# Optimization experiments

Hardware: AMD Instinct MI355X
Metric: run time of the kernel (lower is better)

## Reference

```python
import jax, jax.numpy as jnp
from jax import lax
import numpy as np

FILTER_SIZE = 3
PAD = FILTER_SIZE // 2


def _smooth(off, filt):
    # ReflectionPad2d(pad) -> conv2d(padding=pad) -> crop pad:-pad  == same-size smoothing
    x = jnp.pad(off, ((0, 0), (0, 0), (PAD, PAD), (PAD, PAD)), mode='reflect')
    y = lax.conv_general_dilated(x, filt, window_strides=(1, 1),
                                 padding=[(PAD, PAD), (PAD, PAD)],
                                 dimension_numbers=('NCHW', 'OIHW', 'NCHW'))
    return y[:, :, PAD:-PAD, PAD:-PAD]


def _grid_sample(img, gx, gy):
    # img: [C,H,W]; gx,gy: [N,H,W] normalized to [-1,1].
    # Bilinear, align_corners=True, zero padding (torch 1.x default at repo time).
    C, H, W = img.shape
    ix = (gx + 1.0) * 0.5 * (W - 1)
    iy = (gy + 1.0) * 0.5 * (H - 1)
    x0 = jnp.floor(ix); y0 = jnp.floor(iy)
    x1 = x0 + 1.0;      y1 = y0 + 1.0
    wx1 = ix - x0; wx0 = 1.0 - wx1
    wy1 = iy - y0; wy0 = 1.0 - wy1

    def gather(xi, yi):
        valid = ((xi >= 0) & (xi <= W - 1) & (yi >= 0) & (yi <= H - 1)).astype(img.dtype)
        xc = jnp.clip(xi, 0, W - 1).astype(jnp.int32)
        yc = jnp.clip(yi, 0, H - 1).astype(jnp.int32)
        return img[:, yc, xc] * valid[None]  # [C,N,H,W]

    out = (gather(x0, y0) * (wx0 * wy0)[None] +
           gather(x1, y0) * (wx1 * wy0)[None] +
           gather(x0, y1) * (wx0 * wy1)[None] +
           gather(x1, y1) * (wx1 * wy1)[None])
    return out  # [C,N,H,W]


def setup_inputs() -> dict:
    key = jax.random.key(0)
    k1, k2, k3 = jax.random.split(key, 3)
    C, H, W = 16, 512, 960
    F2 = FILTER_SIZE * FILTER_SIZE
    right_input = jax.random.normal(k1, (1, C, H, W), jnp.float32)
    offset_x = jax.random.uniform(k2, (1, 1, H, W), jnp.float32) * 64.0  # disparity-like
    offset_y = jax.random.uniform(k3, (1, 1, H, W), jnp.float32) * 8.0
    x_coordinate = jnp.tile(jnp.arange(W, dtype=jnp.float32)[None, None, None, :], (1, 1, H, 1))
    y_coordinate = jnp.tile(jnp.arange(H, dtype=jnp.float32)[None, None, :, None], (1, 1, 1, W))
    # one-hot neighbour extraction filters: channel i picks neighbour i of the 3x3 patch
    neighbour_extraction_filter = jnp.eye(F2, dtype=jnp.float32).reshape(F2, 1, FILTER_SIZE, FILTER_SIZE)
    return {'right_input': right_input, 'offset_x': offset_x, 'offset_y': offset_y,
            'x_coordinate': x_coordinate, 'y_coordinate': y_coordinate,
            'neighbour_extraction_filter': neighbour_extraction_filter}


def reference(right_input, offset_x, offset_y, x_coordinate, y_coordinate, neighbour_extraction_filter):
    H, W = offset_x.shape[2], offset_x.shape[3]
    sx = _smooth(offset_x, neighbour_extraction_filter)  # [1,F2,H,W]
    sy = _smooth(offset_y, neighbour_extraction_filter)  # [1,F2,H,W]
    coord_x = jnp.clip(x_coordinate - sx, 0.0, W - 1)
    coord_y = jnp.clip(y_coordinate - sy, 0.0, H - 1)
    half_w = W / 2.0; half_h = H / 2.0
    gx = (coord_x - half_w) / half_w  # [1,F2,H,W]
    gy = (coord_y - half_h) / half_h
    # grid batch = 1*F2; instead of repeating right_input F2 times, gather from the
    # single image for all F2 grids at once, then patch-vote (mean over F2).
    rec = _grid_sample(right_input[0], gx[0], gy[0])  # [C,F2,H,W]
    return jnp.mean(rec, axis=1)[None]  # [1,C,H,W]
```

## Files before the change

kernel.cpp:

```cpp
#include <hip/hip_runtime.h>
#include <hip/hip_fp16.h>

#define CH 16
#define HH 512
#define WW 960
#define HW (HH * WW)

#define TR 8
#define TC 64
#define RROWS 18
#define RCOLS 136
#define NSLOT (RROWS * RCOLS)

typedef __fp16 v2hf __attribute__((ext_vector_type(2)));
typedef _Float16 h2r __attribute__((ext_vector_type(2)));

__device__ __forceinline__ unsigned pkrtz_u(float a, float b) {
  v2hf r = __builtin_amdgcn_cvt_pkrtz(a, b);
  return __builtin_bit_cast(unsigned, r);
}
__device__ __forceinline__ __half2 u2h(unsigned u) {
  return __builtin_bit_cast(__half2, u);
}

__global__ __launch_bounds__(512, 6) void recon_fused_f16(
    const float* __restrict__ img,
    const float* __restrict__ offx,
    const float* __restrict__ offy,
    float* __restrict__ out) {
  __shared__ uint4 lds[NSLOT];

  const int hwid = blockIdx.x + blockIdx.y * 15;
  const int tile = (hwid & 7) * 120 + (hwid >> 3);
  const int tx = tile % 15, ty = tile / 15;
  const int x0b = tx * TC, y0b = ty * TR;
  const int tid = threadIdx.x;
  const int ylo = y0b - 9, xlo = x0b - 68;

  const int pixl = tid & 63;
  const int rowl = tid >> 6;
  const int x = x0b + pixl;
  const int y = y0b + rowl;
  const int po = y * WW + x;

  const float fxs = (float)(WW - 1) / (float)WW;
  const float fys = (float)(HH - 1) / (float)HH;
  const float s = 1.0f / 9.0f;

  int u00a[9];
  __half2 wxa[9];
  __half2 wya[9];
#pragma unroll
  for (int di = -1; di <= 1; ++di) {
    int rr = y + di;
    rr = (rr < 0) ? 1 : ((rr >= HH) ? (HH - 2) : rr);
#pragma unroll
    for (int dj = -1; dj <= 1; ++dj) {
      const int n = (di + 1) * 3 + (dj + 1);
      int cc = x + dj;
      cc = (cc < 0) ? 1 : ((cc >= WW) ? (WW - 2) : cc);
      const int o = rr * WW + cc;
      const float sx = offx[o];
      const float sy = offy[o];
      const float cx = fminf(fmaxf((float)x - sx, 0.0f), (float)(WW - 1));
      const float cy = fminf(fmaxf((float)y - sy, 0.0f), (float)(HH - 1));
      const float ix = cx * fxs;
      const float iy = cy * fys;
      const float fx0 = floorf(ix);
      const float fy0 = floorf(iy);
      const float wx1 = ix - fx0, wx0 = 1.0f - wx1;
      const float wy1 = iy - fy0, wy0 = 1.0f - wy1;
      u00a[n] = ((int)fy0 - ylo) * RCOLS + ((int)fx0 - xlo);
      wxa[n] = u2h(pkrtz_u(wx0 * wy0, wx1 * wy0));
      wya[n] = u2h(pkrtz_u(wx0 * wy1, wx1 * wy1));
    }
  }

#pragma unroll
  for (int chunk = 0; chunk < 2; ++chunk) {
#pragma unroll
    for (int it = 0; it < 5; ++it) {
      const int f = it * 512 + tid;
      if (f < NSLOT) {
        const int row = f / RCOLS;
        const int col = f - row * RCOLS;
        const int gr = min(max(ylo + row, 0), HH - 1);
        const int gc = min(max(xlo + col, 0), WW - 1);
        const float* src = img + (chunk * 8) * HW + gr * WW + gc;
        uint4 o;
        o.x = pkrtz_u(src[0 * HW], src[1 * HW]);
        o.y = pkrtz_u(src[2 * HW], src[3 * HW]);
        o.z = pkrtz_u(src[4 * HW], src[5 * HW]);
        o.w = pkrtz_u(src[6 * HW], src[7 * HW]);
        lds[f] = o;
      }
    }
    __syncthreads();

    float acc[8];
#pragma unroll
    for (int i = 0; i < 8; ++i) acc[i] = 0.f;

#pragma unroll
    for (int di = 0; di < 3; ++di) {
      __half2 h[4];
#pragma unroll
      for (int i = 0; i < 4; ++i) h[i] = u2h(0u);

#pragma unroll
      for (int dj = 0; dj < 3; ++dj) {
        const int n = di * 3 + dj;
        const int u00 = u00a[n];
        const __half2 w00 = __half2half2(__low2half(wxa[n]));
        const __half2 w10 = __half2half2(__high2half(wxa[n]));
        const __half2 w01 = __half2half2(__low2half(wya[n]));
        const __half2 w11 = __half2half2(__high2half(wya[n]));

#define CORNER(UIDX, Wh)                          \
  {                                               \
    const uint4 q = lds[(UIDX)];                  \
    h[0] = __hfma2(u2h(q.x), (Wh), h[0]);         \
    h[1] = __hfma2(u2h(q.y), (Wh), h[1]);         \
    h[2] = __hfma2(u2h(q.z), (Wh), h[2]);         \
    h[3] = __hfma2(u2h(q.w), (Wh), h[3]);         \
  }
        CORNER(u00, w00)
        CORNER(u00 + 1, w10)
        CORNER(u00 + RCOLS, w01)
        CORNER(u00 + RCOLS + 1, w11)
#undef CORNER
      }
#pragma unroll
      for (int i = 0; i < 4; ++i) {
        const h2r a = __builtin_bit_cast(h2r, h[i]);
        acc[2 * i]     += (float)a.x;
        acc[2 * i + 1] += (float)a.y;
      }
    }

#pragma unroll
    for (int j = 0; j < 8; ++j) out[(chunk * 8 + j) * HW + po] = acc[j] * s;

    if (chunk == 0) __syncthreads();
  }
}

extern "C" void kernel_launch(void* const* d_in, const int* in_sizes, int n_in,
                              void* d_out, int out_size, void* d_ws, size_t ws_size,
                              hipStream_t stream) {
  const float* right = (const float*)d_in[0];
  const float* offx  = (const float*)d_in[1];
  const float* offy  = (const float*)d_in[2];
  float* out = (float*)d_out;

  const dim3 grid(WW / TC, HH / TR);
  recon_fused_f16<<<grid, 512, 0, stream>>>(right, offx, offy, out);
}
```

Before: 111.7 us.

## Prefetch second channel chunk into registers while gathering first chunk

Issues the global loads for channels 8-15 into registers (five uint4 per thread) before running the gather for channels 0-7, then writes them to LDS after a barrier. This overlaps the second chunk's global load latency with the first chunk's LDS gather and stores. It also replaces __syncthreads with a custom inline-asm barrier that waits only on lgkmcnt, so outstanding global loads do not have to drain at the barrier. The cost is about 20 extra VGPRs under launch_bounds(512,6), which may cause spills or reduce occupancy.

```diff
diff --git a/kernel.cpp b/kernel.cpp
--- a/kernel.cpp
+++ b/kernel.cpp
@@ -22,6 +22,8 @@
 __device__ __forceinline__ __half2 u2h(unsigned u) {
   return __builtin_bit_cast(__half2, u);
 }
+
+#define LBAR() asm volatile("s_waitcnt lgkmcnt(0)\n\ts_barrier" ::: "memory")
 
 __global__ __launch_bounds__(512, 6) void recon_fused_f16(
     const float* __restrict__ img,
@@ -77,45 +79,57 @@
   }
 
 #pragma unroll
-  for (int chunk = 0; chunk < 2; ++chunk) {
+  for (int it = 0; it < 5; ++it) {
+    const int f = it * 512 + tid;
+    if (f < NSLOT) {
+      const int row = f / RCOLS;
+      const int col = f - row * RCOLS;
+      const int gr = min(max(ylo + row, 0), HH - 1);
+      const int gc = min(max(xlo + col, 0), WW - 1);
+      const float* src = img + gr * WW + gc;
+      uint4 o;
+      o.x = pkrtz_u(src[0 * HW], src[1 * HW]);
+      o.y = pkrtz_u(src[2 * HW], src[3 * HW]);
+      o.z = pkrtz_u(src[4 * HW], src[5 * HW]);
+      o.w = pkrtz_u(src[6 * HW], src[7 * HW]);
+      lds[f] = o;
+    }
+  }
+
+  uint4 p1[5];
 #pragma unroll
-    for (int it = 0; it < 5; ++it) {
-      const int f = it * 512 + tid;
-      if (f < NSLOT) {
-        const int row = f / RCOLS;
-        const int col = f - row * RCOLS;
-        const int gr = min(max(ylo + row, 0), HH - 1);
-        const int gc = min(max(xlo + col, 0), WW - 1);
-        const float* src = img + (chunk * 8) * HW + gr * WW + gc;
-        uint4 o;
-        o.x = pkrtz_u(src[0 * HW], src[1 * HW]);
-        o.y = pkrtz_u(src[2 * HW], src[3 * HW]);
-        o.z = pkrtz_u(src[4 * HW], src[5 * HW]);
-        o.w = pkrtz_u(src[6 * HW], src[7 * HW]);
-        lds[f] = o;
-      }
+  for (int it = 0; it < 5; ++it) {
+    const int f = it * 512 + tid;
+    if (f < NSLOT) {
+      const int row = f / RCOLS;
+      const int col = f - row * RCOLS;
+      const int gr = min(max(ylo + row, 0), HH - 1);
+      const int gc = min(max(xlo + col, 0), WW - 1);
+      const float* src = img + 8 * HW + gr * WW + gc;
+      p1[it].x = pkrtz_u(src[0 * HW], src[1 * HW]);
+      p1[it].y = pkrtz_u(src[2 * HW], src[3 * HW]);
+      p1[it].z = pkrtz_u(src[4 * HW], src[5 * HW]);
+      p1[it].w = pkrtz_u(src[6 * HW], src[7 * HW]);
     }
-    __syncthreads();
+  }
 
+  auto gather_store = [&](int cbase) {
     float acc[8];
 #pragma unroll
     for (int i = 0; i < 8; ++i) acc[i] = 0.f;
-
 #pragma unroll
-    for (int di = 0; di < 3; ++di) {
+    for (int g = 0; g < 3; ++g) {
       __half2 h[4];
 #pragma unroll
       for (int i = 0; i < 4; ++i) h[i] = u2h(0u);
-
 #pragma unroll
       for (int dj = 0; dj < 3; ++dj) {
-        const int n = di * 3 + dj;
+        const int n = g * 3 + dj;
         const int u00 = u00a[n];
         const __half2 w00 = __half2half2(__low2half(wxa[n]));
         const __half2 w10 = __half2half2(__high2half(wxa[n]));
         const __half2 w01 = __half2half2(__low2half(wya[n]));
         const __half2 w11 = __half2half2(__high2half(wya[n]));
-
 #define CORNER(UIDX, Wh)                          \
   {                                               \
     const uint4 q = lds[(UIDX)];                  \
@@ -137,12 +151,21 @@
         acc[2 * i + 1] += (float)a.y;
       }
     }
+#pragma unroll
+    for (int j = 0; j < 8; ++j) out[(cbase + j) * HW + po] = acc[j] * s;
+  };
+
+  LBAR();
+  gather_store(0);
+  LBAR();
 
 #pragma unroll
-    for (int j = 0; j < 8; ++j) out[(chunk * 8 + j) * HW + po] = acc[j] * s;
-
-    if (chunk == 0) __syncthreads();
+  for (int it = 0; it < 5; ++it) {
+    const int f = it * 512 + tid;
+    if (f < NSLOT) lds[f] = p1[it];
   }
+  LBAR();
+  gather_store(8);
 }
 
 extern "C" void kernel_launch(void* const* d_in, const int* in_sizes, int n_in,
```

Result: slower. 117.7 us (+5.4%).
